# Performance work log

Measured on AMD Instinct MI355X. Metric: run time of the kernel, lower is better.

The kernel has to match this reference:

```python
import jax, jax.numpy as jnp
import numpy as np

K = 64                      # sort-pool k
B_GRAPHS, N_PER = 256, 512  # graphs, nodes per graph
DIM_F, E_PER = 128, 8192    # node feature dim, edges per graph
EMB = 32


def setup_inputs() -> dict:
    key = jax.random.key(0)
    ks = jax.random.split(key, 12)
    N = B_GRAPHS * N_PER
    off = (jnp.arange(B_GRAPHS) * N_PER)[:, None]
    x = jax.random.normal(ks[0], (N, DIM_F), jnp.float32)
    edge_src = (jax.random.randint(ks[1], (B_GRAPHS, E_PER), 0, N_PER) + off).reshape(-1)
    edge_dst = (jax.random.randint(ks[2], (B_GRAPHS, E_PER), 0, N_PER) + off).reshape(-1)

    def lin(k, o, i):
        return (jax.random.normal(k, (o, i), jnp.float32) / np.float32(np.sqrt(i)))

    return {
        "x": x,
        "W0": lin(ks[3], EMB, DIM_F), "b0": jnp.zeros((EMB,), jnp.float32),
        "W1": lin(ks[4], EMB, EMB),   "b1": jnp.zeros((EMB,), jnp.float32),
        "W2": lin(ks[5], EMB, EMB),   "b2": jnp.zeros((EMB,), jnp.float32),
        "W3": lin(ks[6], 1, EMB),     "b3": jnp.zeros((1,), jnp.float32),
        "conv1_w": jax.random.normal(ks[7], (16, 1, 97), jnp.float32) / np.float32(np.sqrt(97.0)),
        "conv1_b": jnp.zeros((16,), jnp.float32),
        "conv2_w": jax.random.normal(ks[8], (32, 16, 5), jnp.float32) / np.float32(np.sqrt(80.0)),
        "conv2_b": jnp.zeros((32,), jnp.float32),
        "d1_w": lin(ks[9], 128, 896),  "d1_b": jnp.zeros((128,), jnp.float32),
        "d2_w": lin(ks[10], 10, 128),  "d2_b": jnp.zeros((10,), jnp.float32),
        "edge_src": edge_src, "edge_dst": edge_dst,
        "num_graphs": B_GRAPHS,
    }


def _dgcnn_conv(h_in, W, b, src, dst):
    # h = lin(x); message = (1/deg_src)[dst] * h[src]; scatter-add at dst
    N = h_in.shape[0]
    h = h_in @ W.T + b
    deg = jax.ops.segment_sum(jnp.ones_like(src, dtype=h.dtype), src, num_segments=N)
    norm = 1.0 / deg                       # self-loops guarantee deg >= 1
    msg = h[src] * norm[dst][:, None]      # [E+N, C]
    return jax.ops.segment_sum(msg, dst, num_segments=N)


def _forward(x, W0, b0, W1, b1, W2, b2, W3, b3,
             conv1_w, conv1_b, conv2_w, conv2_b,
             d1_w, d1_b, d2_w, d2_b, src, dst, num_graphs):
    N = x.shape[0]
    self_idx = jnp.arange(N)
    src = jnp.concatenate([src, self_idx])   # add_self_loops
    dst = jnp.concatenate([dst, self_idx])
    hs = []
    h = x
    for (W, b) in ((W0, b0), (W1, b1), (W2, b2), (W3, b3)):
        h = jnp.tanh(_dgcnn_conv(h, W, b, src, dst))
        hs.append(h)
    feat = jnp.concatenate(hs, axis=1)       # [N, 97]
    D = feat.shape[1]
    B = num_graphs
    n = N // B
    g = feat.reshape(B, n, D)
    # global_sort_pool: sort nodes per graph by last channel, descending, take top-k
    order = jnp.argsort(-g[:, :, -1], axis=1)[:, :K]
    topk = jnp.take_along_axis(g, order[:, :, None], axis=1)   # [B, K, D]
    # Conv1d(1,16,kernel=D,stride=D) over [B,1,K*D] == per-node linear on D
    c1 = jax.nn.relu(jnp.einsum('bkd,od->bok', topk, conv1_w[:, 0, :])
                     + conv1_b[None, :, None])                  # [B,16,K]
    p = c1.reshape(B, 16, K // 2, 2).max(axis=-1)               # MaxPool1d(2,2)
    c2 = jax.lax.conv_general_dilated(p, conv2_w, (1,), 'VALID',
                                      dimension_numbers=('NCH', 'OIH', 'NCH'))
    c2 = jax.nn.relu(c2 + conv2_b[None, :, None])               # [B,32,28]
    flat = c2.reshape(B, -1)                                    # [B,896]
    hid = jax.nn.relu(flat @ d1_w.T + d1_b)                     # dropout = identity (eval)
    return hid @ d2_w.T + d2_b                                  # [B,10]


def reference(x, W0, b0, W1, b1, W2, b2, W3, b3,
              conv1_w, conv1_b, conv2_w, conv2_b,
              d1_w, d1_b, d2_w, d2_b, edge_src, edge_dst, num_graphs):
    return _forward(x, W0, b0, W1, b1, W2, b2, W3, b3,
                    conv1_w, conv1_b, conv2_w, conv2_b,
                    d1_w, d1_b, d2_w, d2_b, edge_src, edge_dst, num_graphs)
```

## Files before the change

kernel.cpp:

```cpp
#include <hip/hip_runtime.h>

#define NG   256
#define NP   512
#define EPG  8192
#define FDIM 128
#define STB  36

#define OFF_STAGE 0
#define OFF_BUFB  65536
#define OFF_CSR   139264
#define OFF_OFFS  155648
#define OFF_WT    156680
#define OFF_CUR   156712
#define OFF_DCNT  158760
#define OFF_NRM   160808
#define SMEM_SZ   162856

#define OFF_KEY  OFF_CSR
#define OFF_IDX  (OFF_CSR + 2048)
#define OFF_L3   OFF_CUR
#define FO_FEAT 0
#define FO_C1   6208
#define FO_P    7232
#define FO_C2   7744
#define FO_HID  8640

__global__ __launch_bounds__(1024, 4) void dgcnn_fused(
    const float* __restrict__ x,
    const float* __restrict__ W0, const float* __restrict__ b0,
    const float* __restrict__ W1, const float* __restrict__ b1,
    const float* __restrict__ W2, const float* __restrict__ b2,
    const float* __restrict__ W3, const float* __restrict__ b3,
    const float* __restrict__ c1w, const float* __restrict__ c1b,
    const float* __restrict__ c2w, const float* __restrict__ c2b,
    const float* __restrict__ d1w, const float* __restrict__ d1b,
    const float* __restrict__ d2w, const float* __restrict__ d2b,
    const int* __restrict__ esrc, const int* __restrict__ edst,
    float* __restrict__ hs1, float* __restrict__ hs2,
    float* __restrict__ out)
{
  extern __shared__ char smem[];
  float*          stageF = (float*)(smem + OFF_STAGE);
  float*          bufB  = (float*)(smem + OFF_BUFB);
  unsigned short* csr   = (unsigned short*)(smem + OFF_CSR);
  unsigned short* offs  = (unsigned short*)(smem + OFF_OFFS);
  unsigned int*   wt    = (unsigned int*)(smem + OFF_WT);
  unsigned int*   cur   = (unsigned int*)(smem + OFF_CUR);
  unsigned int*   dcnt  = (unsigned int*)(smem + OFF_DCNT);
  float*          nrm   = (float*)(smem + OFF_NRM);
  float*          lin3S = (float*)(smem + OFF_L3);
  float*          keyA  = (float*)(smem + OFF_KEY);
  unsigned int*   idxA  = (unsigned int*)(smem + OFF_IDX);

  const int g    = blockIdx.x;
  const int tid  = threadIdx.x;
  const int lane = tid & 63;
  const int wv   = __builtin_amdgcn_readfirstlane(tid >> 6);
  const int half = __builtin_amdgcn_readfirstlane(tid >> 9);
  const int v    = tid & 511;
  const int nb   = g * NP;
  const size_t gb = (size_t)g * (NP * 32);

  const int ldRow0 = tid >> 3;
  const int ldGrp  = tid & 7;
  const int ldSwz  = (ldGrp ^ (ldRow0 & 7)) * 16;
  auto load_chunk = [&](int kc, float4* xr) {
    const float* base = x + (size_t)nb * FDIM + kc * 32 + ldGrp * 4;
#pragma unroll
    for (int it = 0; it < 4; it++)
      xr[it] = *(const float4*)(base + (size_t)(ldRow0 + it * 128) * FDIM);
  };
  auto store_chunk = [&](const float4* xr) {
#pragma unroll
    for (int it = 0; it < 4; it++)
      *(float4*)(smem + OFF_STAGE + (ldRow0 + it * 128) * 128 + ldSwz) = xr[it];
  };

  float4 xr[4], xr2[4];
  load_chunk(0, xr);

  if (tid < 512) { cur[tid] = 0u; dcnt[tid] = 0u; }
  __syncthreads();

  int es[8], ed[8];
  {
    const int eb = g * EPG;
    const int4* s4 = (const int4*)(esrc + eb);
    const int4* d4 = (const int4*)(edst + eb);
    const int4 sa = s4[tid], sb = s4[tid + 1024];
    const int4 da = d4[tid], db = d4[tid + 1024];
    es[0]=sa.x-nb; es[1]=sa.y-nb; es[2]=sa.z-nb; es[3]=sa.w-nb;
    es[4]=sb.x-nb; es[5]=sb.y-nb; es[6]=sb.z-nb; es[7]=sb.w-nb;
    ed[0]=da.x-nb; ed[1]=da.y-nb; ed[2]=da.z-nb; ed[3]=da.w-nb;
    ed[4]=db.x-nb; ed[5]=db.y-nb; ed[6]=db.z-nb; ed[7]=db.w-nb;
#pragma unroll
    for (int i = 0; i < 8; i++) {
      atomicAdd(&dcnt[es[i]], 1u);
      atomicAdd(&dcnt[ed[i]], 65536u);
    }
  }
  __syncthreads();

  unsigned c_scan = 0;
  if (tid < 512) {
    const unsigned cw = dcnt[tid];
    nrm[tid] = 1.0f / (float)((cw & 0xFFFFu) + 1u);
    c_scan = cw >> 16;
    for (int d = 1; d < 64; d <<= 1) {
      const unsigned t = __shfl_up(c_scan, (unsigned)d, 64);
      if (lane >= d) c_scan += t;
    }
    if (lane == 63) wt[wv] = c_scan;
  }
  __syncthreads();
  if (tid < 512) {
    unsigned base = 0;
    for (int w = 0; w < wv; w++) base += wt[w];
    offs[tid + 1] = (unsigned short)(base + c_scan);
    if (tid == 0) offs[0] = 0;
  }
  __syncthreads();

#pragma unroll
  for (int i = 0; i < 8; i++) {
    const unsigned pos = (unsigned)offs[ed[i]] + atomicAdd(&cur[ed[i]], 1u);
    csr[pos] = (unsigned short)es[i];
  }

  float acc0[16];
#pragma unroll
  for (int c = 0; c < 16; c++) acc0[c] = b0[half * 16 + c];
  const char* rowp = smem + OFF_STAGE + v * 128;
  const int vswz = v & 7;
  for (int kc = 0; kc < 4; kc++) {
    __syncthreads();
    store_chunk(xr);
    if (kc < 3) load_chunk(kc + 1, xr2);
    __syncthreads();
#pragma unroll
    for (int jg = 0; jg < 8; jg++) {
      const float4 t = *(const float4*)(rowp + ((jg ^ vswz) * 16));
#pragma unroll
      for (int c = 0; c < 16; c++) {
        const float* wr = W0 + (size_t)(half * 16 + c) * FDIM + kc * 32 + jg * 4;
        acc0[c] = fmaf(t.x, wr[0], acc0[c]);
        acc0[c] = fmaf(t.y, wr[1], acc0[c]);
        acc0[c] = fmaf(t.z, wr[2], acc0[c]);
        acc0[c] = fmaf(t.w, wr[3], acc0[c]);
      }
    }
#pragma unroll
    for (int it = 0; it < 4; it++) xr[it] = xr2[it];
  }
  {
    float4* br = (float4*)(bufB + v * STB + half * 16);
#pragma unroll
    for (int j = 0; j < 4; j++)
      br[j] = make_float4(acc0[j*4+0], acc0[j*4+1], acc0[j*4+2], acc0[j*4+3]);
  }
  __syncthreads();

  float h[16];
  auto do_agg = [&]() {
    float4 A0, A1, A2, A3;
    const float4* sr = (const float4*)(bufB + v * STB + half * 16);
    A0 = sr[0]; A1 = sr[1]; A2 = sr[2]; A3 = sr[3];
    const int e0 = offs[v], e1 = offs[v + 1];
    int e = e0;
    for (; e + 1 < e1; e += 2) {
      const int s0 = csr[e], s1 = csr[e + 1];
      const float4* rb0 = (const float4*)(bufB + s0 * STB + half * 16);
      const float4* rb1 = (const float4*)(bufB + s1 * STB + half * 16);
      const float4 p0 = rb0[0], p1 = rb0[1], p2 = rb0[2], p3 = rb0[3];
      const float4 q0 = rb1[0], q1 = rb1[1], q2 = rb1[2], q3 = rb1[3];
      A0.x += p0.x + q0.x; A0.y += p0.y + q0.y; A0.z += p0.z + q0.z; A0.w += p0.w + q0.w;
      A1.x += p1.x + q1.x; A1.y += p1.y + q1.y; A1.z += p1.z + q1.z; A1.w += p1.w + q1.w;
      A2.x += p2.x + q2.x; A2.y += p2.y + q2.y; A2.z += p2.z + q2.z; A2.w += p2.w + q2.w;
      A3.x += p3.x + q3.x; A3.y += p3.y + q3.y; A3.z += p3.z + q3.z; A3.w += p3.w + q3.w;
    }
    if (e < e1) {
      const int s = csr[e];
      const float4* rb = (const float4*)(bufB + s * STB + half * 16);
      const float4 r0 = rb[0], r1 = rb[1], r2 = rb[2], r3 = rb[3];
      A0.x += r0.x; A0.y += r0.y; A0.z += r0.z; A0.w += r0.w;
      A1.x += r1.x; A1.y += r1.y; A1.z += r1.z; A1.w += r1.w;
      A2.x += r2.x; A2.y += r2.y; A2.z += r2.z; A2.w += r2.w;
      A3.x += r3.x; A3.y += r3.y; A3.z += r3.z; A3.w += r3.w;
    }
    const float nv = nrm[v];
    h[0]=tanhf(A0.x*nv); h[1]=tanhf(A0.y*nv); h[2]=tanhf(A0.z*nv); h[3]=tanhf(A0.w*nv);
    h[4]=tanhf(A1.x*nv); h[5]=tanhf(A1.y*nv); h[6]=tanhf(A1.z*nv); h[7]=tanhf(A1.w*nv);
    h[8]=tanhf(A2.x*nv); h[9]=tanhf(A2.y*nv); h[10]=tanhf(A2.z*nv); h[11]=tanhf(A2.w*nv);
    h[12]=tanhf(A3.x*nv); h[13]=tanhf(A3.y*nv); h[14]=tanhf(A3.z*nv); h[15]=tanhf(A3.w*nv);
  };

  auto put_h = [&]() {
    float4* br = (float4*)(bufB + v * STB + half * 16);
#pragma unroll
    for (int j = 0; j < 4; j++)
      br[j] = make_float4(h[j*4+0], h[j*4+1], h[j*4+2], h[j*4+3]);
  };

  auto spill = [&](float* dst) {
#pragma unroll
    for (int c = 0; c < 16; c++)
      dst[gb + (size_t)(half * 16 + c) * 512 + v] = h[c];
  };

  auto do_lin = [&](const float* __restrict__ W, const float* __restrict__ b) {
    float hf[32];
    const float4* rr = (const float4*)(bufB + v * STB);
#pragma unroll
    for (int j = 0; j < 8; j++) {
      const float4 t = rr[j];
      hf[j*4+0]=t.x; hf[j*4+1]=t.y; hf[j*4+2]=t.z; hf[j*4+3]=t.w;
    }
    __syncthreads();
    float acc[16];
#pragma unroll
    for (int c = 0; c < 16; c++) {
      const int C = half * 16 + c;
      const float* wr = W + C * 32;
      float a = b[C];
#pragma unroll
      for (int j = 0; j < 32; j++) a = fmaf(hf[j], wr[j], a);
      acc[c] = a;
    }
    float4* br = (float4*)(bufB + v * STB + half * 16);
#pragma unroll
    for (int j = 0; j < 4; j++)
      br[j] = make_float4(acc[j*4+0], acc[j*4+1], acc[j*4+2], acc[j*4+3]);
    __syncthreads();
  };

  do_agg();
  __syncthreads();
  put_h(); spill(hs1);
  __syncthreads();
  do_lin(W1, b1);
  do_agg();
  __syncthreads();
  put_h(); spill(hs2);
  __syncthreads();
  do_lin(W2, b2);
  do_agg();
  __syncthreads();
  put_h();
  __syncthreads();

  if (tid < 512) {
    const float4* rr = (const float4*)(bufB + tid * STB);
    double a = (double)b3[0];
#pragma unroll
    for (int j = 0; j < 8; j++) {
      const float4 t = rr[j];
      a = fma((double)t.x, (double)W3[j*4+0], a);
      a = fma((double)t.y, (double)W3[j*4+1], a);
      a = fma((double)t.z, (double)W3[j*4+2], a);
      a = fma((double)t.w, (double)W3[j*4+3], a);
    }
    lin3S[tid] = (float)a;
  }
  __syncthreads();
  float h4 = 0.f;
  if (tid < 512) {
    double a = (double)lin3S[tid];
    const int e0 = offs[tid], e1 = offs[tid + 1];
    for (int e = e0; e < e1; e++) a += (double)lin3S[csr[e]];
    a *= (double)nrm[tid];
    h4 = tanhf((float)a);
  }
  __syncthreads();
  if (tid < 512) { keyA[tid] = h4; idxA[tid] = (unsigned)tid; }

  for (int k = 2; k <= NP; k <<= 1) {
    for (int j = k >> 1; j > 0; j >>= 1) {
      __syncthreads();
      if (tid < 512) {
        const int i = tid;
        const int l = i ^ j;
        if (l > i) {
          const float    ki = keyA[i], kl = keyA[l];
          const unsigned ii = idxA[i], il = idxA[l];
          const bool iBeforeL = (ki > kl) || (ki == kl && ii < il);
          const bool doSwap = ((i & k) == 0) ? (!iBeforeL) : iBeforeL;
          if (doSwap) {
            keyA[i] = kl; keyA[l] = ki;
            idxA[i] = il; idxA[l] = ii;
          }
        }
      }
    }
  }
  __syncthreads();

  {
    float* featS = stageF + FO_FEAT;
    const int k = tid >> 4, t = tid & 15;
    const int node = (int)idxA[k];
#pragma unroll
    for (int m = 0; m < 7; m++) {
      const int d = t + 16 * m;
      float val;
      if (d < 32)       val = hs1[gb + (size_t)d * 512 + node];
      else if (d < 64)  val = hs2[gb + (size_t)(d - 32) * 512 + node];
      else if (d < 96)  val = bufB[node * STB + (d - 64)];
      else              val = keyA[k];
      if (d < 97) featS[d * 64 + k] = val;
    }
  }
  __syncthreads();

  {
    const float* featS = stageF + FO_FEAT;
    float* c1s = stageF + FO_C1;
    const int ch = wv;
    double a = (double)c1b[ch];
    const float* wr = c1w + ch * 97;
    for (int d = 0; d < 97; d++)
      a = fma((double)featS[d * 64 + lane], (double)wr[d], a);
    c1s[ch * 64 + lane] = fmaxf((float)a, 0.f);
  }
  __syncthreads();

  if (tid < 512) {
    const float* c1s = stageF + FO_C1;
    float* ps  = stageF + FO_P;
    const int o = tid >> 5, jj = tid & 31;
    ps[o * 32 + jj] = fmaxf(c1s[o * 64 + 2 * jj], c1s[o * 64 + 2 * jj + 1]);
  }
  __syncthreads();

  {
    const float* ps  = stageF + FO_P;
    float* c2s = stageF + FO_C2;
    const int o = wv;
    if (lane < 28) {
      double a0 = 0., a1 = 0.;
      for (int i = 0; i < 16; i++) {
#pragma unroll
        for (int r = 0; r < 5; r++) {
          const double pv = (double)ps[i * 32 + lane + r];
          a0 = fma(pv, (double)c2w[((o     ) * 16 + i) * 5 + r], a0);
          a1 = fma(pv, (double)c2w[((o + 16) * 16 + i) * 5 + r], a1);
        }
      }
      c2s[(o     ) * 28 + lane] = fmaxf((float)(a0 + (double)c2b[o     ]), 0.f);
      c2s[(o + 16) * 28 + lane] = fmaxf((float)(a1 + (double)c2b[o + 16]), 0.f);
    }
  }
  __syncthreads();

  {
    const float* c2s  = stageF + FO_C2;
    float* hids = stageF + FO_HID;
    float fl[14];
#pragma unroll
    for (int j = 0; j < 14; j++) fl[j] = c2s[lane + j * 64];
    for (int hh = 0; hh < 8; hh++) {
      const int hI = wv * 8 + hh;
      const float* wr = d1w + (size_t)hI * 896;
      double a = 0.;
#pragma unroll
      for (int j = 0; j < 14; j++) a = fma((double)fl[j], (double)wr[lane + j * 64], a);
#pragma unroll
      for (int m = 32; m > 0; m >>= 1) a += __shfl_xor(a, m, 64);
      if (lane == 0) hids[hI] = fmaxf((float)(a + (double)d1b[hI]), 0.f);
    }
  }
  __syncthreads();

  if (tid < 10) {
    const float* hids = stageF + FO_HID;
    const float* wr = d2w + tid * 128;
    double a = (double)d2b[tid];
#pragma unroll 8
    for (int hh = 0; hh < 128; hh++) a = fma((double)hids[hh], (double)wr[hh], a);
    out[g * 10 + tid] = (float)a;
  }
}

extern "C" void kernel_launch(void* const* d_in, const int* in_sizes, int n_in,
                              void* d_out, int out_size, void* d_ws, size_t ws_size,
                              hipStream_t stream) {
  const float* x   = (const float*)d_in[0];
  const float* W0  = (const float*)d_in[1];
  const float* b0  = (const float*)d_in[2];
  const float* W1  = (const float*)d_in[3];
  const float* b1  = (const float*)d_in[4];
  const float* W2  = (const float*)d_in[5];
  const float* b2  = (const float*)d_in[6];
  const float* W3  = (const float*)d_in[7];
  const float* b3  = (const float*)d_in[8];
  const float* c1w = (const float*)d_in[9];
  const float* c1b = (const float*)d_in[10];
  const float* c2w = (const float*)d_in[11];
  const float* c2b = (const float*)d_in[12];
  const float* d1w = (const float*)d_in[13];
  const float* d1b = (const float*)d_in[14];
  const float* d2w = (const float*)d_in[15];
  const float* d2b = (const float*)d_in[16];
  const int* esrc  = (const int*)d_in[17];
  const int* edst  = (const int*)d_in[18];

  float* hs1 = (float*)d_ws;
  float* hs2 = hs1 + (size_t)NG * NP * 32;
  float* outp = (float*)d_out;

  hipFuncSetAttribute(reinterpret_cast<const void*>(dgcnn_fused),
                      hipFuncAttributeMaxDynamicSharedMemorySize, SMEM_SZ);
  dgcnn_fused<<<NG, 1024, SMEM_SZ, stream>>>(x, W0, b0, W1, b1, W2, b2, W3, b3,
                                             c1w, c1b, c2w, c2b, d1w, d1b, d2w, d2b,
                                             esrc, edst, hs1, hs2, outp);
}
```

Baseline: 282.7 us.

## Replace bitonic sort with rank-count top-k and keep layer-1 features in LDS

The 45-step bitonic sort over 512 keys, with a barrier per step, is replaced by a parallel rank computation: each node counts how many keys beat it across two halves, and nodes ranked below 64 write their index directly. Layer-1 hidden states now stay in the LDS stage buffer instead of being spilled to global memory. Layer-2 spills are written row-major as float4 so the top-k gather reads contiguous rows. The edge-index global loads are also hoisted ahead of the x load and barrier. This costs O(N^2) comparisons per graph instead of a sort, and it depends on the stage region not being overwritten between layer 1 and the gather.

```diff
diff --git a/kernel.cpp b/kernel.cpp
--- a/kernel.cpp
+++ b/kernel.cpp
@@ -16,9 +16,11 @@
 #define OFF_NRM   160808
 #define SMEM_SZ   162856
 
-#define OFF_KEY  OFF_CSR
-#define OFF_IDX  (OFF_CSR + 2048)
-#define OFF_L3   OFF_CUR
+#define OFF_KEY   OFF_CSR
+#define OFF_RANKP (OFF_CSR + 2048)
+#define OFF_TIDX  (OFF_CSR + 4096)
+#define OFF_TKEY  (OFF_CSR + 4352)
+#define OFF_L3    OFF_CUR
 #define FO_FEAT 0
 #define FO_C1   6208
 #define FO_P    7232
@@ -36,7 +38,7 @@
     const float* __restrict__ d1w, const float* __restrict__ d1b,
     const float* __restrict__ d2w, const float* __restrict__ d2b,
     const int* __restrict__ esrc, const int* __restrict__ edst,
-    float* __restrict__ hs1, float* __restrict__ hs2,
+    float* __restrict__ hs2,
     float* __restrict__ out)
 {
   extern __shared__ char smem[];
@@ -50,7 +52,9 @@
   float*          nrm   = (float*)(smem + OFF_NRM);
   float*          lin3S = (float*)(smem + OFF_L3);
   float*          keyA  = (float*)(smem + OFF_KEY);
-  unsigned int*   idxA  = (unsigned int*)(smem + OFF_IDX);
+  unsigned short* rankP = (unsigned short*)(smem + OFF_RANKP);
+  unsigned short* topIdx= (unsigned short*)(smem + OFF_TIDX);
+  float*          topKey= (float*)(smem + OFF_TKEY);
 
   const int g    = blockIdx.x;
   const int tid  = threadIdx.x;
@@ -59,7 +63,6 @@
   const int half = __builtin_amdgcn_readfirstlane(tid >> 9);
   const int v    = tid & 511;
   const int nb   = g * NP;
-  const size_t gb = (size_t)g * (NP * 32);
 
   const int ldRow0 = tid >> 3;
   const int ldGrp  = tid & 7;
@@ -76,6 +79,11 @@
       *(float4*)(smem + OFF_STAGE + (ldRow0 + it * 128) * 128 + ldSwz) = xr[it];
   };
 
+  const int eb = g * EPG;
+  const int4* s4p = (const int4*)(esrc + eb);
+  const int4* d4p = (const int4*)(edst + eb);
+  const int4 sa = s4p[tid], sb = s4p[tid + 1024];
+  const int4 da = d4p[tid], db = d4p[tid + 1024];
   float4 xr[4], xr2[4];
   load_chunk(0, xr);
 
@@ -84,11 +92,6 @@
 
   int es[8], ed[8];
   {
-    const int eb = g * EPG;
-    const int4* s4 = (const int4*)(esrc + eb);
-    const int4* d4 = (const int4*)(edst + eb);
-    const int4 sa = s4[tid], sb = s4[tid + 1024];
-    const int4 da = d4[tid], db = d4[tid + 1024];
     es[0]=sa.x-nb; es[1]=sa.y-nb; es[2]=sa.z-nb; es[3]=sa.w-nb;
     es[4]=sb.x-nb; es[5]=sb.y-nb; es[6]=sb.z-nb; es[7]=sb.w-nb;
     ed[0]=da.x-nb; ed[1]=da.y-nb; ed[2]=da.z-nb; ed[3]=da.w-nb;
@@ -201,10 +204,17 @@
       br[j] = make_float4(h[j*4+0], h[j*4+1], h[j*4+2], h[j*4+3]);
   };
 
-  auto spill = [&](float* dst) {
+  auto store_h1 = [&]() {
 #pragma unroll
     for (int c = 0; c < 16; c++)
-      dst[gb + (size_t)(half * 16 + c) * 512 + v] = h[c];
+      stageF[(half * 16 + c) * 512 + v] = h[c];
+  };
+
+  auto spill2 = [&]() {
+    float4* dst = (float4*)(hs2 + (size_t)(nb + v) * 32 + half * 16);
+#pragma unroll
+    for (int j = 0; j < 4; j++)
+      dst[j] = make_float4(h[j*4+0], h[j*4+1], h[j*4+2], h[j*4+3]);
   };
 
   auto do_lin = [&](const float* __restrict__ W, const float* __restrict__ b) {
@@ -235,12 +245,12 @@
 
   do_agg();
   __syncthreads();
-  put_h(); spill(hs1);
+  put_h(); store_h1();
   __syncthreads();
   do_lin(W1, b1);
   do_agg();
   __syncthreads();
-  put_h(); spill(hs2);
+  put_h(); spill2();
   __syncthreads();
   do_lin(W2, b2);
   do_agg();
@@ -271,49 +281,61 @@
     h4 = tanhf((float)a);
   }
   __syncthreads();
-  if (tid < 512) { keyA[tid] = h4; idxA[tid] = (unsigned)tid; }
-
-  for (int k = 2; k <= NP; k <<= 1) {
-    for (int j = k >> 1; j > 0; j >>= 1) {
-      __syncthreads();
-      if (tid < 512) {
-        const int i = tid;
-        const int l = i ^ j;
-        if (l > i) {
-          const float    ki = keyA[i], kl = keyA[l];
-          const unsigned ii = idxA[i], il = idxA[l];
-          const bool iBeforeL = (ki > kl) || (ki == kl && ii < il);
-          const bool doSwap = ((i & k) == 0) ? (!iBeforeL) : iBeforeL;
-          if (doSwap) {
-            keyA[i] = kl; keyA[l] = ki;
-            idxA[i] = il; idxA[l] = ii;
-          }
-        }
-      }
-    }
-  }
-  __syncthreads();
-
-  {
-    float* featS = stageF + FO_FEAT;
-    const int k = tid >> 4, t = tid & 15;
-    const int node = (int)idxA[k];
-#pragma unroll
-    for (int m = 0; m < 7; m++) {
-      const int d = t + 16 * m;
-      float val;
-      if (d < 32)       val = hs1[gb + (size_t)d * 512 + node];
-      else if (d < 64)  val = hs2[gb + (size_t)(d - 32) * 512 + node];
-      else if (d < 96)  val = bufB[node * STB + (d - 64)];
-      else              val = keyA[k];
-      if (d < 97) featS[d * 64 + k] = val;
-    }
-  }
-  __syncthreads();
-
-  {
-    const float* featS = stageF + FO_FEAT;
-    float* c1s = stageF + FO_C1;
+  if (tid < 512) keyA[tid] = h4;
+  __syncthreads();
+
+  {
+    const int i = tid & 511;
+    const int p = tid >> 9;
+    const float ki = keyA[i];
+    const float4* k4 = (const float4*)(keyA + p * 256);
+    int cnt = 0;
+#pragma unroll 8
+    for (int jj = 0; jj < 64; jj++) {
+      const float4 kv = k4[jj];
+      const int j0 = p * 256 + jj * 4;
+      cnt += (kv.x > ki || (kv.x == ki && (j0    ) < i)) ? 1 : 0;
+      cnt += (kv.y > ki || (kv.y == ki && (j0 + 1) < i)) ? 1 : 0;
+      cnt += (kv.z > ki || (kv.z == ki && (j0 + 2) < i)) ? 1 : 0;
+      cnt += (kv.w > ki || (kv.w == ki && (j0 + 3) < i)) ? 1 : 0;
+    }
+    rankP[tid] = (unsigned short)cnt;
+  }
+  __syncthreads();
+  if (tid < 512) {
+    const int r = (int)rankP[tid] + (int)rankP[tid + 512];
+    if (r < 64) { topIdx[r] = (unsigned short)tid; topKey[r] = keyA[tid]; }
+  }
+  __syncthreads();
+
+  {
+    const int k = lane;
+    const int t = wv;
+    const int node = (int)topIdx[k];
+    const float a0 = stageF[ t       * 512 + node];
+    const float a1 = stageF[(t + 16) * 512 + node];
+    const float* h2row = hs2 + (size_t)(nb + node) * 32;
+    const float b0v = h2row[t];
+    const float b1v = h2row[t + 16];
+    const float* brow = bufB + node * STB;
+    const float c0v = brow[t];
+    const float c1v = brow[t + 16];
+    const float kk = topKey[k];
+    __syncthreads();
+    float* featS = bufB + FO_FEAT;
+    featS[ t        * 64 + k] = a0;
+    featS[(t + 16)  * 64 + k] = a1;
+    featS[(t + 32)  * 64 + k] = b0v;
+    featS[(t + 48)  * 64 + k] = b1v;
+    featS[(t + 64)  * 64 + k] = c0v;
+    featS[(t + 80)  * 64 + k] = c1v;
+    if (t == 0) featS[96 * 64 + k] = kk;
+  }
+  __syncthreads();
+
+  {
+    const float* featS = bufB + FO_FEAT;
+    float* c1s = bufB + FO_C1;
     const int ch = wv;
     double a = (double)c1b[ch];
     const float* wr = c1w + ch * 97;
@@ -324,16 +346,16 @@
   __syncthreads();
 
   if (tid < 512) {
-    const float* c1s = stageF + FO_C1;
-    float* ps  = stageF + FO_P;
+    const float* c1s = bufB + FO_C1;
+    float* ps  = bufB + FO_P;
     const int o = tid >> 5, jj = tid & 31;
     ps[o * 32 + jj] = fmaxf(c1s[o * 64 + 2 * jj], c1s[o * 64 + 2 * jj + 1]);
   }
   __syncthreads();
 
   {
-    const float* ps  = stageF + FO_P;
-    float* c2s = stageF + FO_C2;
+    const float* ps  = bufB + FO_P;
+    float* c2s = bufB + FO_C2;
     const int o = wv;
     if (lane < 28) {
       double a0 = 0., a1 = 0.;
@@ -352,8 +374,8 @@
   __syncthreads();
 
   {
-    const float* c2s  = stageF + FO_C2;
-    float* hids = stageF + FO_HID;
+    const float* c2s  = bufB + FO_C2;
+    float* hids = bufB + FO_HID;
     float fl[14];
 #pragma unroll
     for (int j = 0; j < 14; j++) fl[j] = c2s[lane + j * 64];
@@ -371,7 +393,7 @@
   __syncthreads();
 
   if (tid < 10) {
-    const float* hids = stageF + FO_HID;
+    const float* hids = bufB + FO_HID;
     const float* wr = d2w + tid * 128;
     double a = (double)d2b[tid];
 #pragma unroll 8
@@ -403,13 +425,12 @@
   const int* esrc  = (const int*)d_in[17];
   const int* edst  = (const int*)d_in[18];
 
-  float* hs1 = (float*)d_ws;
-  float* hs2 = hs1 + (size_t)NG * NP * 32;
+  float* hs2 = (float*)d_ws;
   float* outp = (float*)d_out;
 
   hipFuncSetAttribute(reinterpret_cast<const void*>(dgcnn_fused),
                       hipFuncAttributeMaxDynamicSharedMemorySize, SMEM_SZ);
   dgcnn_fused<<<NG, 1024, SMEM_SZ, stream>>>(x, W0, b0, W1, b1, W2, b2, W3, b3,
                                              c1w, c1b, c2w, c2b, d1w, d1b, d2w, d2b,
-                                             esrc, edst, hs1, hs2, outp);
+                                             esrc, edst, hs2, outp);
 }
```

New measurement: 285.4 us. No clear change (+1.0%).
